# Kernel tuning notes

Measured on AMD Instinct MI355X. Metric: run time of the kernel, lower is better.

## Reference

```python
import jax, jax.numpy as jnp
import numpy as np

B, S, T = 2048, 32, 32
D, H = 128, 256       # cle_dim, rnn_dim
VS, VT = 256, 256     # source/target char vocab
BOW = 1               # MorphoDataset.Factor.BOW


def setup_inputs() -> dict:
    key = jax.random.key(0)
    ks = jax.random.split(key, 16)
    n = lambda k, sh: (jax.random.normal(k, sh, jnp.float32) * 0.05)
    inp = {
        "src_emb": n(ks[0], (VS, D)),
        "tgt_emb": n(ks[1], (VT, D)),
        "enc_f_W": n(ks[2], (D, 3 * H)),
        "enc_f_U": n(ks[3], (H, 3 * H)),
        "enc_f_b": jnp.zeros((2, 3 * H), jnp.float32),
        "enc_b_W": n(ks[4], (D, 3 * H)),
        "enc_b_U": n(ks[5], (H, 3 * H)),
        "enc_b_b": jnp.zeros((2, 3 * H), jnp.float32),
        "dec_W": n(ks[6], (D + H, 3 * H)),
        "dec_U": n(ks[7], (H, 3 * H)),
        "dec_b": jnp.zeros((2, 3 * H), jnp.float32),
        "out_W": n(ks[8], (H, VT)),
        "out_b": jnp.zeros((VT,), jnp.float32),
        "att_src_W": n(ks[9], (H, H)),
        "att_src_b": jnp.zeros((H,), jnp.float32),
        "att_st_W": n(ks[10], (H, H)),
        "att_st_b": jnp.zeros((H,), jnp.float32),
        "att_v": n(ks[11], (H, 1)),
        "att_v_b": jnp.zeros((1,), jnp.float32),
        "source_ids": jax.random.randint(ks[12], (B, S), 0, VS, jnp.int32),
        "target_ids": jax.random.randint(ks[13], (B, T), 0, VT, jnp.int32),
    }
    return inp


def _gru_step(h, x, W, U, b):
    # Keras GRU, reset_after=True: separate input/recurrent biases b[0], b[1]
    gx = x @ W + b[0]
    gh = h @ U + b[1]
    xz, xr, xh = jnp.split(gx, 3, axis=-1)
    hz, hr, hh = jnp.split(gh, 3, axis=-1)
    z = jax.nn.sigmoid(xz + hz)
    r = jax.nn.sigmoid(xr + hr)
    c = jnp.tanh(xh + r * hh)
    return z * h + (1.0 - z) * c


def _gru_scan(x_tbd, W, U, b):
    # x_tbd: [S, B, D] -> outputs [S, B, H]
    h0 = jnp.zeros((x_tbd.shape[1], U.shape[0]), x_tbd.dtype)
    def step(h, x):
        h = _gru_step(h, x, W, U, b)
        return h, h
    _, ys = jax.lax.scan(step, h0, x_tbd)
    return ys


def reference(src_emb, tgt_emb, enc_f_W, enc_f_U, enc_f_b, enc_b_W, enc_b_U, enc_b_b,
              dec_W, dec_U, dec_b, out_W, out_b, att_src_W, att_src_b,
              att_st_W, att_st_b, att_v, att_v_b, source_ids, target_ids):
    # ---- Encoder: bidirectional GRU, merge_mode='sum' ----
    x = src_emb[source_ids]                      # [B, S, D]
    x_t = jnp.transpose(x, (1, 0, 2))            # [S, B, D]
    fwd = _gru_scan(x_t, enc_f_W, enc_f_U, enc_f_b)
    bwd = _gru_scan(x_t[::-1], enc_b_W, enc_b_U, enc_b_b)[::-1]
    source_states = jnp.transpose(fwd + bwd, (1, 0, 2))  # [B, S, H]

    # projected source states are constant across decoder steps -> precompute
    proj_src = source_states @ att_src_W + att_src_b     # [B, S, H]

    def attend(inp, h):
        p = h @ att_st_W + att_st_b                      # [B, H]
        e = jnp.tanh(proj_src + p[:, None, :]) @ att_v + att_v_b  # [B, S, 1]
        w = jax.nn.softmax(e, axis=1)                    # softmax over source positions
        ctx = jnp.sum(source_states * w, axis=1)         # [B, H]
        return jnp.concatenate([inp, ctx], axis=1)       # [B, D+H]

    # ---- Decoder (teacher forcing) ----
    h0 = source_states[:, 0]                             # [B, H]
    bow = jnp.broadcast_to(tgt_emb[BOW], (source_ids.shape[0], tgt_emb.shape[1]))
    inp0 = attend(bow, h0)

    def dstep(carry, tgt_t):
        h, inp = carry
        h = _gru_step(h, inp, dec_W, dec_U, dec_b)       # GRUCell step
        logits = h @ out_W + out_b                       # [B, VT]
        nxt = attend(tgt_emb[tgt_t], h)
        return (h, nxt), logits

    _, logits = jax.lax.scan(dstep, (h0, inp0), jnp.transpose(target_ids))
    return jnp.transpose(logits, (1, 0, 2))              # [B, T, VT]
```

## Files before the change

kernel.cpp:

```cpp
#include <hip/hip_runtime.h>
#include <math.h>

#define B_  2048
#define S_  32
#define T_  32
#define D_  128
#define H_  256
#define G3  768
#define VT_ 256
#define BOW_ 1

typedef __attribute__((ext_vector_type(8))) short short8;
typedef __attribute__((ext_vector_type(4))) float f32x4;
typedef __attribute__((ext_vector_type(4))) unsigned short us4;
typedef __attribute__((ext_vector_type(8))) unsigned short us8;
typedef unsigned short u16;

__device__ inline u16 f2bf(float x) {
  union { float f; unsigned u; } v; v.f = x;
  unsigned r = v.u + 0x7FFFu + ((v.u >> 16) & 1u);
  return (u16)(r >> 16);
}
__device__ inline float bf2f(u16 b) {
  union { unsigned u; float f; } v; v.u = ((unsigned)b) << 16; return v.f;
}
__device__ inline int swz(int r) { return ((r ^ (r >> 3)) & 7) << 3; }
__device__ inline float sigm(float x) { return 1.f / (1.f + expf(-x)); }

struct TMat { const float* src; u16* dhi; u16* dlo; int R; int C; int tile0; };
struct TPack { TMat m[10]; };

__global__ __launch_bounds__(256)
void wsplit_t(TPack P) {
  int bx = blockIdx.x;
  TMat M = P.m[0];
  #pragma unroll
  for (int i = 1; i < 10; i++) if (bx >= P.m[i].tile0) M = P.m[i];
  int ti = bx - M.tile0;
  int tilesR = M.R >> 6;
  int rt = ti % tilesR, ct = ti / tilesR;
  int r0 = rt * 64, c0 = ct * 64;
  __shared__ float ts[64][65];
  int tid = threadIdx.x;
  int cx = tid & 63, ry = tid >> 6;
  #pragma unroll
  for (int i = 0; i < 16; i++) {
    int r = ry * 16 + i;
    ts[r][cx] = M.src[(size_t)(r0 + r) * M.C + c0 + cx];
  }
  __syncthreads();
  int rx = tid & 63, cy = tid >> 6;
  #pragma unroll
  for (int i = 0; i < 16; i++) {
    int cc = cy * 16 + i;
    float v = ts[rx][cc];
    u16 hi = f2bf(v);
    size_t o = (size_t)(c0 + cc) * M.R + r0 + rx;
    M.dhi[o] = hi;
    M.dlo[o] = f2bf(v - bf2f(hi));
  }
}

__global__ __launch_bounds__(256)
void esplit(const float* a, const float* b, u16* ah, u16* al, u16* bh, u16* bl, int n) {
  int i = blockIdx.x * 256 + threadIdx.x;
  if (i >= 2 * n) return;
  const float* s = (i < n) ? a : b;
  u16* dh = (i < n) ? ah : bh;
  u16* dl = (i < n) ? al : bl;
  int j = (i < n) ? i : i - n;
  float v = s[j];
  u16 hi = f2bf(v);
  dh[j] = hi; dl[j] = f2bf(v - bf2f(hi));
}

struct PLeg {
  const u16* Ahi; const u16* Alo; const float* Af32; int lda;
  const u16* Bthi; const u16* Btlo; int ldb;
  const float* bias; void* C; int ldc; int cmode;
  int M, N, K;
};

__global__ __launch_bounds__(256)
void gemm_pl(PLeg l0, PLeg l1) {
  PLeg L = blockIdx.z ? l1 : l0;
  int n0 = blockIdx.x * 128; if (n0 >= L.N) return;
  int m0 = blockIdx.y * 128; if (m0 >= L.M) return;
  __shared__ u16 As[128 * 64];
  __shared__ u16 Bs[128 * 64];
  int tid = threadIdx.x;
  int lane = tid & 63, wv = tid >> 6;
  int wr = (wv >> 1) * 64, wc = (wv & 1) * 64;
  int fr = lane & 15, fk = (lane >> 4) * 8;
  f32x4 acc[4][4];
  #pragma unroll
  for (int m = 0; m < 4; m++)
    #pragma unroll
    for (int n = 0; n < 4; n++) acc[m][n] = (f32x4){0.f, 0.f, 0.f, 0.f};

  int s_row = tid >> 1, s_part = tid & 1;

  for (int k0 = 0; k0 < L.K; k0 += 32) {
    if (k0) __syncthreads();
    int swA = swz(s_row);
    if (L.Af32) {
      const float* src = L.Af32 + (size_t)(m0 + s_row) * L.lda + k0 + s_part * 16;
      #pragma unroll
      for (int q = 0; q < 4; q++) {
        f32x4 v = *(const f32x4*)(src + q * 4);
        us4 hv, lv;
        #pragma unroll
        for (int j = 0; j < 4; j++) {
          u16 h = f2bf(v[j]); hv[j] = h; lv[j] = f2bf(v[j] - bf2f(h));
        }
        *(us4*)&As[(s_row * 64 + s_part * 16 + q * 4) ^ swA]      = hv;
        *(us4*)&As[(s_row * 64 + 32 + s_part * 16 + q * 4) ^ swA] = lv;
      }
    } else {
      const u16* src = (s_part ? L.Alo : L.Ahi) + (size_t)(m0 + s_row) * L.lda + k0;
      #pragma unroll
      for (int q = 0; q < 4; q++)
        *(us8*)&As[(s_row * 64 + s_part * 32 + q * 8) ^ swA] = *(const us8*)(src + q * 8);
    }
    {
      const u16* src = (s_part ? L.Btlo : L.Bthi) + (size_t)(n0 + s_row) * L.ldb + k0;
      #pragma unroll
      for (int q = 0; q < 4; q++)
        *(us8*)&Bs[(s_row * 64 + s_part * 32 + q * 8) ^ swA] = *(const us8*)(src + q * 8);
    }
    __syncthreads();
    short8 bhi[4], blo[4];
    #pragma unroll
    for (int n = 0; n < 4; n++) {
      int c = wc + n * 16 + fr; int sw = swz(c);
      bhi[n] = *(const short8*)&Bs[(c * 64 + fk) ^ sw];
      blo[n] = *(const short8*)&Bs[(c * 64 + 32 + fk) ^ sw];
    }
    #pragma unroll
    for (int m = 0; m < 4; m++) {
      int r = wr + m * 16 + fr; int sw = swz(r);
      short8 ahi = *(const short8*)&As[(r * 64 + fk) ^ sw];
      short8 alo = *(const short8*)&As[(r * 64 + 32 + fk) ^ sw];
      #pragma unroll
      for (int n = 0; n < 4; n++) {
        acc[m][n] = __builtin_amdgcn_mfma_f32_16x16x32_bf16(ahi, bhi[n], acc[m][n], 0, 0, 0);
        acc[m][n] = __builtin_amdgcn_mfma_f32_16x16x32_bf16(ahi, blo[n], acc[m][n], 0, 0, 0);
        acc[m][n] = __builtin_amdgcn_mfma_f32_16x16x32_bf16(alo, bhi[n], acc[m][n], 0, 0, 0);
      }
    }
  }
  int rbase = (lane >> 4) * 4;
  #pragma unroll
  for (int m = 0; m < 4; m++)
    #pragma unroll
    for (int rr = 0; rr < 4; rr++) {
      int row = m0 + wr + m * 16 + rbase + rr;
      #pragma unroll
      for (int n = 0; n < 4; n++) {
        int col = n0 + wc + n * 16 + fr;
        float v = acc[m][n][rr];
        if (L.bias) v += L.bias[col];
        if (L.cmode == 0) ((float*)L.C)[(size_t)row * L.ldc + col] = v;
        else              ((u16*)L.C)[(size_t)row * L.ldc + col] = f2bf(v);
      }
    }
}

struct Seg {
  const u16* Ahi; const u16* Alo; int lda;
  const u16* Bthi; const u16* Btlo; int ldb;
  int K; int gmode;
};
struct StepDesc {
  Seg seg[3]; int nseg;
  const float* b0; const float* b1;
  const float* hold; float* hnew;
  u16* hh; u16* hl;
  float* ssf; int ssmode;
  u16* ss0h; u16* ss0l; int writeSS0;
  const int* ids; int sidx;
};

__global__ __launch_bounds__(256)
void gru_step(StepDesc d0, StepDesc d1) {
  StepDesc D = blockIdx.z ? d1 : d0;
  int j0 = blockIdx.x * 64;
  int m0 = blockIdx.y * 64;
  __shared__ u16 As[64 * 64];
  __shared__ u16 Bs[3 * 64 * 64];
  int tid = threadIdx.x;
  int lane = tid & 63, wv = tid >> 6;
  int wr = (wv >> 1) * 32, wc = (wv & 1) * 32;
  int fr = lane & 15, fk = (lane >> 4) * 8;
  f32x4 acc[4][2][2];
  #pragma unroll
  for (int a = 0; a < 4; a++)
    #pragma unroll
    for (int m = 0; m < 2; m++)
      #pragma unroll
      for (int n = 0; n < 2; n++) acc[a][m][n] = (f32x4){0.f, 0.f, 0.f, 0.f};

  int a_row = tid >> 2, a_part = (tid >> 1) & 1, a_half = tid & 1;

  #pragma unroll
  for (int sg = 0; sg < 3; sg++) {
    if (sg < D.nseg) {
      Seg S = D.seg[sg];
      int grow = m0 + a_row;
      int arow;
      if (S.gmode == 0)      arow = grow;
      else if (S.gmode == 1) arow = D.ids[grow * S_ + D.sidx];
      else if (S.gmode == 2) arow = D.ids[grow * S_ + (S_ - 1 - D.sidx)];
      else                   arow = (D.sidx == 0) ? BOW_ : D.ids[grow * T_ + D.sidx - 1];
      const u16* Ap = a_part ? S.Alo : S.Ahi;
      for (int k0 = 0; k0 < S.K; k0 += 32) {
        if (!(sg == 0 && k0 == 0)) __syncthreads();
        {
          int sw = swz(a_row);
          const u16* src = Ap + (size_t)arow * S.lda + k0 + a_half * 16;
          int bse = a_row * 64 + a_part * 32 + a_half * 16;
          *(us8*)&As[(bse + 0) ^ sw] = *(const us8*)(src);
          *(us8*)&As[(bse + 8) ^ sw] = *(const us8*)(src + 8);
        }
        #pragma unroll
        for (int st = 0; st < 3; st++) {
          int n768 = st * H_ + j0 + a_row;
          const u16* srcB = (a_part ? S.Btlo : S.Bthi) + (size_t)n768 * S.ldb + k0 + a_half * 16;
          int sw = swz(a_row);
          int bse = a_row * 64 + a_part * 32 + a_half * 16;
          *(us8*)&Bs[st * 4096 + ((bse + 0) ^ sw)] = *(const us8*)(srcB);
          *(us8*)&Bs[st * 4096 + ((bse + 8) ^ sw)] = *(const us8*)(srcB + 8);
        }
        __syncthreads();
        short8 ah[2], al[2];
        #pragma unroll
        for (int m = 0; m < 2; m++) {
          int r = wr + m * 16 + fr; int sw = swz(r);
          ah[m] = *(const short8*)&As[(r * 64 + fk) ^ sw];
          al[m] = *(const short8*)&As[(r * 64 + 32 + fk) ^ sw];
        }
        #pragma unroll
        for (int st = 0; st < 3; st++) {
          int ai = (st < 2) ? st : (sg == 0 ? 2 : 3);
          #pragma unroll
          for (int n = 0; n < 2; n++) {
            int c = wc + n * 16 + fr; int sw = swz(c);
            short8 bh = *(const short8*)&Bs[st * 4096 + ((c * 64 + fk) ^ sw)];
            short8 bl = *(const short8*)&Bs[st * 4096 + ((c * 64 + 32 + fk) ^ sw)];
            #pragma unroll
            for (int m = 0; m < 2; m++) {
              acc[ai][m][n] = __builtin_amdgcn_mfma_f32_16x16x32_bf16(ah[m], bh, acc[ai][m][n], 0, 0, 0);
              acc[ai][m][n] = __builtin_amdgcn_mfma_f32_16x16x32_bf16(ah[m], bl, acc[ai][m][n], 0, 0, 0);
              acc[ai][m][n] = __builtin_amdgcn_mfma_f32_16x16x32_bf16(al[m], bh, acc[ai][m][n], 0, 0, 0);
            }
          }
        }
      }
    }
  }

  int rbase = (lane >> 4) * 4;
  #pragma unroll
  for (int m = 0; m < 2; m++)
    #pragma unroll
    for (int rr = 0; rr < 4; rr++) {
      int b = m0 + wr + m * 16 + rbase + rr;
      #pragma unroll
      for (int n = 0; n < 2; n++) {
        int j = j0 + wc + n * 16 + fr;
        float az  = acc[0][m][n][rr];
        float ar  = acc[1][m][n][rr];
        float ahc = acc[2][m][n][rr];
        float axc = acc[3][m][n][rr];
        float z = sigm(az + D.b0[j] + D.b1[j]);
        float r = sigm(ar + D.b0[H_ + j] + D.b1[H_ + j]);
        float c = tanhf(axc + D.b0[2 * H_ + j] + r * (ahc + D.b1[2 * H_ + j]));
        size_t o = (size_t)b * H_ + j;
        float hn = z * D.hold[o] + (1.f - z) * c;
        D.hnew[o] = hn;
        u16 hi = f2bf(hn);
        D.hh[o] = hi; D.hl[o] = f2bf(hn - bf2f(hi));
        if (D.ssmode == 1) {
          D.ssf[o] = hn;
        } else if (D.ssmode == 2) {
          float v = D.ssf[o] + hn;
          D.ssf[o] = v;
          if (D.writeSS0) {
            u16 vh = f2bf(v);
            D.ss0h[o] = vh; D.ss0l[o] = f2bf(v - bf2f(vh));
          }
        }
      }
    }
}

__global__ __launch_bounds__(256)
void attend_k(const u16* __restrict__ projbf, const float* __restrict__ ss,
              const float* __restrict__ p, const float* __restrict__ att_v,
              u16* __restrict__ ctxh, u16* __restrict__ ctxl) {
  int b = blockIdx.x;
  int tid = threadIdx.x;
  int lane = tid & 63;
  int wv = tid >> 6;
  __shared__ float e_s[S_];
  __shared__ float w_s[S_];
  float pq[4], vq[4];
  #pragma unroll
  for (int q = 0; q < 4; q++) {
    pq[q] = p[(size_t)b * H_ + q * 64 + lane];
    vq[q] = att_v[q * 64 + lane];
  }
  #pragma unroll
  for (int i = 0; i < 8; i++) {
    int s = wv * 8 + i;
    const u16* pr = projbf + ((size_t)s * B_ + b) * H_;
    float part = 0.f;
    #pragma unroll
    for (int q = 0; q < 4; q++)
      part += tanhf(bf2f(pr[q * 64 + lane]) + pq[q]) * vq[q];
    #pragma unroll
    for (int off = 32; off; off >>= 1)
      part += __shfl_xor(part, off);
    if (lane == 0) e_s[s] = part;
  }
  __syncthreads();
  float m = -1e30f;
  #pragma unroll
  for (int s = 0; s < S_; s++) m = fmaxf(m, e_s[s]);
  float den = 0.f;
  #pragma unroll
  for (int s = 0; s < S_; s++) den += expf(e_s[s] - m);
  if (tid < S_) w_s[tid] = expf(e_s[tid] - m) / den;
  __syncthreads();
  float acc = 0.f;
  #pragma unroll
  for (int s = 0; s < S_; s++)
    acc = fmaf(w_s[s], ss[((size_t)s * B_ + b) * H_ + tid], acc);
  u16 hi = f2bf(acc);
  size_t o = (size_t)b * H_ + tid;
  ctxh[o] = hi; ctxl[o] = f2bf(acc - bf2f(hi));
}

extern "C" void kernel_launch(void* const* d_in, const int* in_sizes, int n_in,
                              void* d_out, int out_size, void* d_ws, size_t ws_size,
                              hipStream_t stream) {
  const float* src_emb   = (const float*)d_in[0];
  const float* tgt_emb   = (const float*)d_in[1];
  const float* enc_f_W   = (const float*)d_in[2];
  const float* enc_f_U   = (const float*)d_in[3];
  const float* enc_f_b   = (const float*)d_in[4];
  const float* enc_b_W   = (const float*)d_in[5];
  const float* enc_b_U   = (const float*)d_in[6];
  const float* enc_b_b   = (const float*)d_in[7];
  const float* dec_W     = (const float*)d_in[8];
  const float* dec_U     = (const float*)d_in[9];
  const float* dec_b     = (const float*)d_in[10];
  const float* out_W     = (const float*)d_in[11];
  const float* out_b     = (const float*)d_in[12];
  const float* att_src_W = (const float*)d_in[13];
  const float* att_src_b = (const float*)d_in[14];
  const float* att_st_W  = (const float*)d_in[15];
  const float* att_st_b  = (const float*)d_in[16];
  const float* att_v     = (const float*)d_in[17];
  const int* source_ids  = (const int*)d_in[19];
  const int* target_ids  = (const int*)d_in[20];
  float* out = (float*)d_out;

  char* base = (char*)d_ws;
  size_t off = 0;
  auto allocB = [&](size_t bytes) { void* p = base + off; off = (off + bytes + 255) & ~255UL; return p; };
  const size_t BH = (size_t)B_ * H_;

  float* ss    = (float*)allocB((size_t)S_ * BH * 4);
  u16*  projbf = (u16*) allocB((size_t)S_ * BH * 2);
  float* pbuf  = (float*)allocB(BH * 4);
  u16* ctxh = (u16*)allocB(BH * 2);
  u16* ctxl = (u16*)allocB(BH * 2);
  u16* ss0h = (u16*)allocB(BH * 2);
  u16* ss0l = (u16*)allocB(BH * 2);
  float* hEncF[2][2]; u16* hEncH[2][2]; u16* hEncL[2][2];
  for (int d = 0; d < 2; d++)
    for (int p = 0; p < 2; p++) {
      hEncF[d][p] = (float*)allocB(BH * 4);
      hEncH[d][p] = (u16*)allocB(BH * 2);
      hEncL[d][p] = (u16*)allocB(BH * 2);
    }
  float* hDecF[2]; u16* hDecH[2]; u16* hDecL[2];
  for (int p = 0; p < 2; p++) {
    hDecF[p] = (float*)allocB(BH * 4);
    hDecH[p] = (u16*)allocB(BH * 2);
    hDecL[p] = (u16*)allocB(BH * 2);
  }
  auto planes2 = [&](size_t n, u16*& h, u16*& l) { h = (u16*)allocB(n * 2); l = (u16*)allocB(n * 2); };
  u16 *UtFh,*UtFl,*UtBh,*UtBl,*WtFh,*WtFl,*WtBh,*WtBl;
  u16 *dUth,*dUtl,*dWcth,*dWctl,*dWxth,*dWxtl;
  u16 *oWth,*oWtl,*aStth,*aSttl,*aSrth,*aSrtl;
  u16 *sEh,*sEl,*tEh,*tEl;
  planes2((size_t)G3*H_, UtFh, UtFl);   planes2((size_t)G3*H_, UtBh, UtBl);
  planes2((size_t)G3*D_, WtFh, WtFl);   planes2((size_t)G3*D_, WtBh, WtBl);
  planes2((size_t)G3*H_, dUth, dUtl);   planes2((size_t)G3*H_, dWcth, dWctl);
  planes2((size_t)G3*D_, dWxth, dWxtl);
  planes2((size_t)H_*VT_, oWth, oWtl);
  planes2((size_t)H_*H_, aStth, aSttl); planes2((size_t)H_*H_, aSrth, aSrtl);
  planes2((size_t)VT_*D_, sEh, sEl);    planes2((size_t)VT_*D_, tEh, tEl);

  TPack P;
  P.m[0] = { enc_f_U,            UtFh, UtFl, 256, 768, 0   };
  P.m[1] = { enc_b_U,            UtBh, UtBl, 256, 768, 48  };
  P.m[2] = { dec_U,              dUth, dUtl, 256, 768, 96  };
  P.m[3] = { dec_W + 128 * G3,   dWcth, dWctl, 256, 768, 144 };
  P.m[4] = { enc_f_W,            WtFh, WtFl, 128, 768, 192 };
  P.m[5] = { enc_b_W,            WtBh, WtBl, 128, 768, 216 };
  P.m[6] = { dec_W,              dWxth, dWxtl, 128, 768, 240 };
  P.m[7] = { out_W,              oWth, oWtl, 256, 256, 264 };
  P.m[8] = { att_st_W,           aStth, aSttl, 256, 256, 280 };
  P.m[9] = { att_src_W,          aSrth, aSrtl, 256, 256, 296 };
  wsplit_t<<<312, 256, 0, stream>>>(P);
  esplit<<<(2 * VT_ * D_ + 255) / 256, 256, 0, stream>>>(src_emb, tgt_emb, sEh, sEl, tEh, tEl, VT_ * D_);

  for (int d = 0; d < 2; d++) {
    hipMemsetAsync(hEncF[d][0], 0, BH * 4, stream);
    hipMemsetAsync(hEncH[d][0], 0, BH * 2, stream);
    hipMemsetAsync(hEncL[d][0], 0, BH * 2, stream);
  }

  for (int s = 0; s < S_; s++) {
    int p = s & 1;
    StepDesc dd[2];
    for (int d = 0; d < 2; d++) {
      StepDesc& D = dd[d];
      D.seg[0] = { hEncH[d][p], hEncL[d][p], H_, d ? UtBh : UtFh, d ? UtBl : UtFl, H_, H_, 0 };
      D.seg[1] = { sEh, sEl, D_, d ? WtBh : WtFh, d ? WtBl : WtFl, D_, D_, d ? 2 : 1 };
      D.seg[2] = D.seg[1];
      D.nseg = 2;
      D.b0 = d ? enc_b_b : enc_f_b;
      D.b1 = (d ? enc_b_b : enc_f_b) + G3;
      D.hold = hEncF[d][p]; D.hnew = hEncF[d][p ^ 1];
      D.hh = hEncH[d][p ^ 1]; D.hl = hEncL[d][p ^ 1];
      int pos = d ? (S_ - 1 - s) : s;
      D.ssf = ss + (size_t)pos * BH;
      D.ssmode = (s < S_ / 2) ? 1 : 2;
      D.ss0h = ss0h; D.ss0l = ss0l;
      D.writeSS0 = (d == 1 && s == S_ - 1) ? 1 : 0;
      D.ids = source_ids; D.sidx = s;
    }
    gru_step<<<dim3(4, 32, 2), 256, 0, stream>>>(dd[0], dd[1]);
  }

  {
    PLeg proj = { nullptr, nullptr, ss, H_, aSrth, aSrtl, H_, att_src_b,
                  projbf, H_, 1, S_ * B_, H_, H_ };
    PLeg p0   = { nullptr, nullptr, ss, H_, aStth, aSttl, H_, att_st_b,
                  pbuf, H_, 0, B_, H_, H_ };
    gemm_pl<<<dim3(2, 512, 2), 256, 0, stream>>>(proj, p0);
  }
  attend_k<<<B_, 256, 0, stream>>>(projbf, ss, pbuf, att_v, ctxh, ctxl);

  for (int t = 0; t < T_; t++) {
    int p = t & 1;
    StepDesc D;
    D.seg[0] = { t ? hDecH[p] : ss0h, t ? hDecL[p] : ss0l, H_, dUth, dUtl, H_, H_, 0 };
    D.seg[1] = { ctxh, ctxl, H_, dWcth, dWctl, H_, H_, 0 };
    D.seg[2] = { tEh, tEl, D_, dWxth, dWxtl, D_, D_, 3 };
    D.nseg = 3;
    D.b0 = dec_b; D.b1 = dec_b + G3;
    D.hold = t ? hDecF[p] : ss;
    D.hnew = hDecF[p ^ 1];
    D.hh = hDecH[p ^ 1]; D.hl = hDecL[p ^ 1];
    D.ssf = nullptr; D.ssmode = 0;
    D.ss0h = nullptr; D.ss0l = nullptr; D.writeSS0 = 0;
    D.ids = target_ids; D.sidx = t;
    gru_step<<<dim3(4, 32, 1), 256, 0, stream>>>(D, D);

    PLeg LO = { hDecH[p ^ 1], hDecL[p ^ 1], nullptr, H_, oWth, oWtl, H_, out_b,
                out + (size_t)t * VT_, T_ * VT_, 0, B_, VT_, H_ };
    PLeg LP = { hDecH[p ^ 1], hDecL[p ^ 1], nullptr, H_, aStth, aSttl, H_, att_st_b,
                pbuf, H_, 0, B_, H_, H_ };
    gemm_pl<<<dim3(2, 16, 2), 256, 0, stream>>>(LO, LP);

    if (t < T_ - 1)
      attend_k<<<B_, 256, 0, stream>>>(projbf, ss, pbuf, att_v, ctxh, ctxl);
  }
}
```

Measured before the change: 4.048 ms.

## Restructure GRU step kernel and batch decoder output projection after the loop

The GRU step kernel now stages the whole concatenated A operand (hidden state, context and embedding rows) in shared memory once, with 32-row tiles. B weights are streamed directly from global memory instead of being staged per k-chunk through LDS, which removes most barriers. Source states are kept as bf16 hi/lo planes instead of fp32. All decoder hidden states are stored so the output logits projection runs as one large GEMM after the loop rather than once per step. This cuts per-step launch work and synchronisation, but B loads now hit global or cache memory with no LDS reuse, and attention now uses only the bf16 high part of the source states, which lowers its precision.

```diff
diff --git a/kernel.cpp b/kernel.cpp
--- a/kernel.cpp
+++ b/kernel.cpp
@@ -12,7 +12,6 @@
 
 typedef __attribute__((ext_vector_type(8))) short short8;
 typedef __attribute__((ext_vector_type(4))) float f32x4;
-typedef __attribute__((ext_vector_type(4))) unsigned short us4;
 typedef __attribute__((ext_vector_type(8))) unsigned short us8;
 typedef unsigned short u16;
 
@@ -75,7 +74,7 @@
 }
 
 struct PLeg {
-  const u16* Ahi; const u16* Alo; const float* Af32; int lda;
+  const u16* Ahi; const u16* Alo; int lda;
   const u16* Bthi; const u16* Btlo; int ldb;
   const float* bias; void* C; int ldc; int cmode;
   int M, N, K;
@@ -103,20 +102,7 @@
   for (int k0 = 0; k0 < L.K; k0 += 32) {
     if (k0) __syncthreads();
     int swA = swz(s_row);
-    if (L.Af32) {
-      const float* src = L.Af32 + (size_t)(m0 + s_row) * L.lda + k0 + s_part * 16;
-      #pragma unroll
-      for (int q = 0; q < 4; q++) {
-        f32x4 v = *(const f32x4*)(src + q * 4);
-        us4 hv, lv;
-        #pragma unroll
-        for (int j = 0; j < 4; j++) {
-          u16 h = f2bf(v[j]); hv[j] = h; lv[j] = f2bf(v[j] - bf2f(h));
-        }
-        *(us4*)&As[(s_row * 64 + s_part * 16 + q * 4) ^ swA]      = hv;
-        *(us4*)&As[(s_row * 64 + 32 + s_part * 16 + q * 4) ^ swA] = lv;
-      }
-    } else {
+    {
       const u16* src = (s_part ? L.Alo : L.Ahi) + (size_t)(m0 + s_row) * L.lda + k0;
       #pragma unroll
       for (int q = 0; q < 4; q++)
@@ -160,142 +146,159 @@
         int col = n0 + wc + n * 16 + fr;
         float v = acc[m][n][rr];
         if (L.bias) v += L.bias[col];
-        if (L.cmode == 0) ((float*)L.C)[(size_t)row * L.ldc + col] = v;
-        else              ((u16*)L.C)[(size_t)row * L.ldc + col] = f2bf(v);
-      }
-    }
-}
-
-struct Seg {
-  const u16* Ahi; const u16* Alo; int lda;
-  const u16* Bthi; const u16* Btlo; int ldb;
-  int K; int gmode;
+        if (L.cmode == 0)      ((float*)L.C)[(size_t)row * L.ldc + col] = v;
+        else if (L.cmode == 1) ((u16*)L.C)[(size_t)row * L.ldc + col] = f2bf(v);
+        else {
+          size_t o = (((size_t)(row & (B_ - 1))) * T_ + (row >> 11)) * VT_ + col;
+          ((float*)L.C)[o] = v;
+        }
+      }
+    }
+}
+
+struct GruDesc {
+  const u16 *a0H, *a0L;
+  const u16 *a1H, *a1L;
+  const u16 *a2H, *a2L;
+  const u16 *b0H, *b0L;
+  const u16 *b1H, *b1L;
+  const u16 *b2H, *b2L;
+  const float *bias0, *bias1;
+  const float *hold;
+  const u16 *holdH, *holdL;
+  float *hnew;
+  u16 *hh, *hl;
+  u16 *ssH, *ssL;
+  const int *ids;
+  int ssmode;
+  int sidx, rev;
 };
-struct StepDesc {
-  Seg seg[3]; int nseg;
-  const float* b0; const float* b1;
-  const float* hold; float* hnew;
-  u16* hh; u16* hl;
-  float* ssf; int ssmode;
-  u16* ss0h; u16* ss0l; int writeSS0;
-  const int* ids; int sidx;
-};
-
+
+template<int MODE>
 __global__ __launch_bounds__(256)
-void gru_step(StepDesc d0, StepDesc d1) {
-  StepDesc D = blockIdx.z ? d1 : d0;
+void gru_step(GruDesc d0, GruDesc d1) {
+  GruDesc D = blockIdx.z ? d1 : d0;
+  constexpr int KT  = MODE ? 640 : 384;
+  constexpr int KT8 = KT / 8;
+  __shared__ u16 As[2 * 32 * KT];
+
   int j0 = blockIdx.x * 64;
-  int m0 = blockIdx.y * 64;
-  __shared__ u16 As[64 * 64];
-  __shared__ u16 Bs[3 * 64 * 64];
+  int m0 = blockIdx.y * 32;
   int tid = threadIdx.x;
   int lane = tid & 63, wv = tid >> 6;
-  int wr = (wv >> 1) * 32, wc = (wv & 1) * 32;
-  int fr = lane & 15, fk = (lane >> 4) * 8;
-  f32x4 acc[4][2][2];
+  int fr = lane & 15, kq = lane >> 4;
+  int jn = j0 + wv * 16 + fr;
+
+  constexpr int SLOTS = 2 * 32 * KT8;
+  constexpr int PER_T = SLOTS / 256;
+  #pragma unroll
+  for (int i = 0; i < PER_T; i++) {
+    int s = tid + i * 256;
+    int p = s / (32 * KT8);
+    int rem = s - p * (32 * KT8);
+    int row = rem / KT8;
+    int kb = rem - row * KT8;
+    int k = kb * 8;
+    const u16* src;
+    if (MODE == 0) {
+      if (k < 256) src = (p ? D.a0L : D.a0H) + (size_t)(m0 + row) * 256 + k;
+      else {
+        int ar = D.ids[(m0 + row) * S_ + (D.rev ? (S_ - 1 - D.sidx) : D.sidx)];
+        src = (p ? D.a1L : D.a1H) + (size_t)ar * 128 + (k - 256);
+      }
+    } else {
+      if (k < 256)      src = (p ? D.a0L : D.a0H) + (size_t)(m0 + row) * 256 + k;
+      else if (k < 512) src = (p ? D.a1L : D.a1H) + (size_t)(m0 + row) * 256 + (k - 256);
+      else {
+        int ar = (D.sidx == 0) ? BOW_ : D.ids[(m0 + row) * T_ + D.sidx - 1];
+        src = (p ? D.a2L : D.a2H) + (size_t)ar * 128 + (k - 512);
+      }
+    }
+    *(us8*)&As[(s ^ (row & 7)) * 8] = *(const us8*)src;
+  }
+  __syncthreads();
+
+  f32x4 acc[4][2];
   #pragma unroll
   for (int a = 0; a < 4; a++)
     #pragma unroll
-    for (int m = 0; m < 2; m++)
+    for (int m = 0; m < 2; m++) acc[a][m] = (f32x4){0.f, 0.f, 0.f, 0.f};
+
+  int arow_slot[2];
+  #pragma unroll
+  for (int m = 0; m < 2; m++) arow_slot[m] = (m * 16 + fr) * KT8 + kq;
+
+  auto kstep = [&](int k0, int bk, const u16* bHp, const u16* bLp, int ldb, int ai2) {
+    short8 ah[2], al[2];
+    #pragma unroll
+    for (int m = 0; m < 2; m++) {
+      int sl = (arow_slot[m] + (k0 >> 3)) ^ (fr & 7);
+      ah[m] = *(const short8*)&As[sl * 8];
+      sl = (arow_slot[m] + 32 * KT8 + (k0 >> 3)) ^ (fr & 7);
+      al[m] = *(const short8*)&As[sl * 8];
+    }
+    #pragma unroll
+    for (int st = 0; st < 3; st++) {
+      size_t ro = (size_t)(st * 256 + jn) * ldb + bk + kq * 8;
+      short8 bh = *(const short8*)(bHp + ro);
+      short8 bl = *(const short8*)(bLp + ro);
+      int ai = (st < 2) ? st : ai2;
       #pragma unroll
-      for (int n = 0; n < 2; n++) acc[a][m][n] = (f32x4){0.f, 0.f, 0.f, 0.f};
-
-  int a_row = tid >> 2, a_part = (tid >> 1) & 1, a_half = tid & 1;
-
-  #pragma unroll
-  for (int sg = 0; sg < 3; sg++) {
-    if (sg < D.nseg) {
-      Seg S = D.seg[sg];
-      int grow = m0 + a_row;
-      int arow;
-      if (S.gmode == 0)      arow = grow;
-      else if (S.gmode == 1) arow = D.ids[grow * S_ + D.sidx];
-      else if (S.gmode == 2) arow = D.ids[grow * S_ + (S_ - 1 - D.sidx)];
-      else                   arow = (D.sidx == 0) ? BOW_ : D.ids[grow * T_ + D.sidx - 1];
-      const u16* Ap = a_part ? S.Alo : S.Ahi;
-      for (int k0 = 0; k0 < S.K; k0 += 32) {
-        if (!(sg == 0 && k0 == 0)) __syncthreads();
-        {
-          int sw = swz(a_row);
-          const u16* src = Ap + (size_t)arow * S.lda + k0 + a_half * 16;
-          int bse = a_row * 64 + a_part * 32 + a_half * 16;
-          *(us8*)&As[(bse + 0) ^ sw] = *(const us8*)(src);
-          *(us8*)&As[(bse + 8) ^ sw] = *(const us8*)(src + 8);
+      for (int m = 0; m < 2; m++) {
+        acc[ai][m] = __builtin_amdgcn_mfma_f32_16x16x32_bf16(ah[m], bh, acc[ai][m], 0, 0, 0);
+        acc[ai][m] = __builtin_amdgcn_mfma_f32_16x16x32_bf16(ah[m], bl, acc[ai][m], 0, 0, 0);
+        acc[ai][m] = __builtin_amdgcn_mfma_f32_16x16x32_bf16(al[m], bh, acc[ai][m], 0, 0, 0);
+      }
+    }
+  };
+
+  #pragma unroll
+  for (int k0 = 0; k0 < 256; k0 += 32) kstep(k0, k0, D.b0H, D.b0L, 256, 2);
+  if (MODE == 0) {
+    #pragma unroll
+    for (int k0 = 256; k0 < 384; k0 += 32) kstep(k0, k0 - 256, D.b1H, D.b1L, 128, 3);
+  } else {
+    #pragma unroll
+    for (int k0 = 256; k0 < 512; k0 += 32) kstep(k0, k0 - 256, D.b1H, D.b1L, 256, 3);
+    #pragma unroll
+    for (int k0 = 512; k0 < 640; k0 += 32) kstep(k0, k0 - 512, D.b2H, D.b2L, 128, 3);
+  }
+
+  int rbase = kq * 4;
+  int j = jn;
+  float bz = D.bias0[j] + D.bias1[j];
+  float br = D.bias0[H_ + j] + D.bias1[H_ + j];
+  float bxc = D.bias0[2 * H_ + j];
+  float bhc = D.bias1[2 * H_ + j];
+  #pragma unroll
+  for (int m = 0; m < 2; m++)
+    #pragma unroll
+    for (int rr = 0; rr < 4; rr++) {
+      int b = m0 + m * 16 + rbase + rr;
+      size_t o = (size_t)b * H_ + j;
+      float z = sigm(acc[0][m][rr] + bz);
+      float r = sigm(acc[1][m][rr] + br);
+      float c = tanhf(acc[3][m][rr] + bxc + r * (acc[2][m][rr] + bhc));
+      float hprev = D.hold ? D.hold[o] : (bf2f(D.holdH[o]) + bf2f(D.holdL[o]));
+      float hn = z * hprev + (1.f - z) * c;
+      D.hnew[o] = hn;
+      u16 hi = f2bf(hn);
+      D.hh[o] = hi; D.hl[o] = f2bf(hn - bf2f(hi));
+      if (MODE == 0) {
+        if (D.ssmode == 1) {
+          u16 vh = f2bf(hn);
+          D.ssH[o] = vh; D.ssL[o] = f2bf(hn - bf2f(vh));
+        } else if (D.ssmode == 2) {
+          float v = bf2f(D.ssH[o]) + bf2f(D.ssL[o]) + hn;
+          u16 vh = f2bf(v);
+          D.ssH[o] = vh; D.ssL[o] = f2bf(v - bf2f(vh));
         }
-        #pragma unroll
-        for (int st = 0; st < 3; st++) {
-          int n768 = st * H_ + j0 + a_row;
-          const u16* srcB = (a_part ? S.Btlo : S.Bthi) + (size_t)n768 * S.ldb + k0 + a_half * 16;
-          int sw = swz(a_row);
-          int bse = a_row * 64 + a_part * 32 + a_half * 16;
-          *(us8*)&Bs[st * 4096 + ((bse + 0) ^ sw)] = *(const us8*)(srcB);
-          *(us8*)&Bs[st * 4096 + ((bse + 8) ^ sw)] = *(const us8*)(srcB + 8);
-        }
-        __syncthreads();
-        short8 ah[2], al[2];
-        #pragma unroll
-        for (int m = 0; m < 2; m++) {
-          int r = wr + m * 16 + fr; int sw = swz(r);
-          ah[m] = *(const short8*)&As[(r * 64 + fk) ^ sw];
-          al[m] = *(const short8*)&As[(r * 64 + 32 + fk) ^ sw];
-        }
-        #pragma unroll
-        for (int st = 0; st < 3; st++) {
-          int ai = (st < 2) ? st : (sg == 0 ? 2 : 3);
-          #pragma unroll
-          for (int n = 0; n < 2; n++) {
-            int c = wc + n * 16 + fr; int sw = swz(c);
-            short8 bh = *(const short8*)&Bs[st * 4096 + ((c * 64 + fk) ^ sw)];
-            short8 bl = *(const short8*)&Bs[st * 4096 + ((c * 64 + 32 + fk) ^ sw)];
-            #pragma unroll
-            for (int m = 0; m < 2; m++) {
-              acc[ai][m][n] = __builtin_amdgcn_mfma_f32_16x16x32_bf16(ah[m], bh, acc[ai][m][n], 0, 0, 0);
-              acc[ai][m][n] = __builtin_amdgcn_mfma_f32_16x16x32_bf16(ah[m], bl, acc[ai][m][n], 0, 0, 0);
-              acc[ai][m][n] = __builtin_amdgcn_mfma_f32_16x16x32_bf16(al[m], bh, acc[ai][m][n], 0, 0, 0);
-            }
-          }
-        }
-      }
-    }
-  }
-
-  int rbase = (lane >> 4) * 4;
-  #pragma unroll
-  for (int m = 0; m < 2; m++)
-    #pragma unroll
-    for (int rr = 0; rr < 4; rr++) {
-      int b = m0 + wr + m * 16 + rbase + rr;
-      #pragma unroll
-      for (int n = 0; n < 2; n++) {
-        int j = j0 + wc + n * 16 + fr;
-        float az  = acc[0][m][n][rr];
-        float ar  = acc[1][m][n][rr];
-        float ahc = acc[2][m][n][rr];
-        float axc = acc[3][m][n][rr];
-        float z = sigm(az + D.b0[j] + D.b1[j]);
-        float r = sigm(ar + D.b0[H_ + j] + D.b1[H_ + j]);
-        float c = tanhf(axc + D.b0[2 * H_ + j] + r * (ahc + D.b1[2 * H_ + j]));
-        size_t o = (size_t)b * H_ + j;
-        float hn = z * D.hold[o] + (1.f - z) * c;
-        D.hnew[o] = hn;
-        u16 hi = f2bf(hn);
-        D.hh[o] = hi; D.hl[o] = f2bf(hn - bf2f(hi));
-        if (D.ssmode == 1) {
-          D.ssf[o] = hn;
-        } else if (D.ssmode == 2) {
-          float v = D.ssf[o] + hn;
-          D.ssf[o] = v;
-          if (D.writeSS0) {
-            u16 vh = f2bf(v);
-            D.ss0h[o] = vh; D.ss0l[o] = f2bf(v - bf2f(vh));
-          }
-        }
       }
     }
 }
 
 __global__ __launch_bounds__(256)
-void attend_k(const u16* __restrict__ projbf, const float* __restrict__ ss,
+void attend_k(const u16* __restrict__ projbf, const u16* __restrict__ ssH,
               const float* __restrict__ p, const float* __restrict__ att_v,
               u16* __restrict__ ctxh, u16* __restrict__ ctxl) {
   int b = blockIdx.x;
@@ -335,7 +338,7 @@
   float acc = 0.f;
   #pragma unroll
   for (int s = 0; s < S_; s++)
-    acc = fmaf(w_s[s], ss[((size_t)s * B_ + b) * H_ + tid], acc);
+    acc = fmaf(w_s[s], bf2f(ssH[((size_t)s * B_ + b) * H_ + tid]), acc);
   u16 hi = f2bf(acc);
   size_t o = (size_t)b * H_ + tid;
   ctxh[o] = hi; ctxl[o] = f2bf(acc - bf2f(hi));
@@ -371,26 +374,25 @@
   auto allocB = [&](size_t bytes) { void* p = base + off; off = (off + bytes + 255) & ~255UL; return p; };
   const size_t BH = (size_t)B_ * H_;
 
-  float* ss    = (float*)allocB((size_t)S_ * BH * 4);
-  u16*  projbf = (u16*) allocB((size_t)S_ * BH * 2);
-  float* pbuf  = (float*)allocB(BH * 4);
+  u16* ssH    = (u16*)allocB((size_t)S_ * BH * 2);
+  u16* ssL    = (u16*)allocB((size_t)S_ * BH * 2);
+  u16* projbf = (u16*)allocB((size_t)S_ * BH * 2);
+  float* pbuf = (float*)allocB(BH * 4);
   u16* ctxh = (u16*)allocB(BH * 2);
   u16* ctxl = (u16*)allocB(BH * 2);
-  u16* ss0h = (u16*)allocB(BH * 2);
-  u16* ss0l = (u16*)allocB(BH * 2);
-  float* hEncF[2][2]; u16* hEncH[2][2]; u16* hEncL[2][2];
-  for (int d = 0; d < 2; d++)
-    for (int p = 0; p < 2; p++) {
-      hEncF[d][p] = (float*)allocB(BH * 4);
-      hEncH[d][p] = (u16*)allocB(BH * 2);
-      hEncL[d][p] = (u16*)allocB(BH * 2);
-    }
-  float* hDecF[2]; u16* hDecH[2]; u16* hDecL[2];
-  for (int p = 0; p < 2; p++) {
-    hDecF[p] = (float*)allocB(BH * 4);
-    hDecH[p] = (u16*)allocB(BH * 2);
-    hDecL[p] = (u16*)allocB(BH * 2);
-  }
+
+  float* encF0 = (float*)allocB(2 * BH * 4);
+  u16*  encPl0 = (u16*)allocB(4 * BH * 2);
+  float* encF1 = (float*)allocB(2 * BH * 4);
+  u16*  encPl1 = (u16*)allocB(4 * BH * 2);
+  float* encF[2][2]  = { { encF0, encF0 + BH }, { encF1, encF1 + BH } };
+  u16*  encH[2][2]   = { { encPl0, encPl0 + 2 * BH }, { encPl1, encPl1 + 2 * BH } };
+  u16*  encL[2][2]   = { { encPl0 + BH, encPl0 + 3 * BH }, { encPl1 + BH, encPl1 + 3 * BH } };
+
+  float* hDecF[2] = { (float*)allocB(BH * 4), (float*)allocB(BH * 4) };
+  u16* hAllH = (u16*)allocB((size_t)T_ * BH * 2);
+  u16* hAllL = (u16*)allocB((size_t)T_ * BH * 2);
+
   auto planes2 = [&](size_t n, u16*& h, u16*& l) { h = (u16*)allocB(n * 2); l = (u16*)allocB(n * 2); };
   u16 *UtFh,*UtFl,*UtBh,*UtBl,*WtFh,*WtFl,*WtBh,*WtBl;
   u16 *dUth,*dUtl,*dWcth,*dWctl,*dWxth,*dWxtl;
@@ -405,80 +407,84 @@
   planes2((size_t)VT_*D_, sEh, sEl);    planes2((size_t)VT_*D_, tEh, tEl);
 
   TPack P;
-  P.m[0] = { enc_f_U,            UtFh, UtFl, 256, 768, 0   };
-  P.m[1] = { enc_b_U,            UtBh, UtBl, 256, 768, 48  };
-  P.m[2] = { dec_U,              dUth, dUtl, 256, 768, 96  };
-  P.m[3] = { dec_W + 128 * G3,   dWcth, dWctl, 256, 768, 144 };
-  P.m[4] = { enc_f_W,            WtFh, WtFl, 128, 768, 192 };
-  P.m[5] = { enc_b_W,            WtBh, WtBl, 128, 768, 216 };
-  P.m[6] = { dec_W,              dWxth, dWxtl, 128, 768, 240 };
-  P.m[7] = { out_W,              oWth, oWtl, 256, 256, 264 };
-  P.m[8] = { att_st_W,           aStth, aSttl, 256, 256, 280 };
-  P.m[9] = { att_src_W,          aSrth, aSrtl, 256, 256, 296 };
+  P.m[0] = { enc_f_U,          UtFh, UtFl, 256, 768, 0   };
+  P.m[1] = { enc_b_U,          UtBh, UtBl, 256, 768, 48  };
+  P.m[2] = { dec_U,            dUth, dUtl, 256, 768, 96  };
+  P.m[3] = { dec_W + 128 * G3, dWcth, dWctl, 256, 768, 144 };
+  P.m[4] = { enc_f_W,          WtFh, WtFl, 128, 768, 192 };
+  P.m[5] = { enc_b_W,          WtBh, WtBl, 128, 768, 216 };
+  P.m[6] = { dec_W,            dWxth, dWxtl, 128, 768, 240 };
+  P.m[7] = { out_W,            oWth, oWtl, 256, 256, 264 };
+  P.m[8] = { att_st_W,         aStth, aSttl, 256, 256, 280 };
+  P.m[9] = { att_src_W,        aSrth, aSrtl, 256, 256, 296 };
   wsplit_t<<<312, 256, 0, stream>>>(P);
   esplit<<<(2 * VT_ * D_ + 255) / 256, 256, 0, stream>>>(src_emb, tgt_emb, sEh, sEl, tEh, tEl, VT_ * D_);
 
-  for (int d = 0; d < 2; d++) {
-    hipMemsetAsync(hEncF[d][0], 0, BH * 4, stream);
-    hipMemsetAsync(hEncH[d][0], 0, BH * 2, stream);
-    hipMemsetAsync(hEncL[d][0], 0, BH * 2, stream);
-  }
+  hipMemsetAsync(encF0, 0, 2 * BH * 4, stream);
+  hipMemsetAsync(encPl0, 0, 4 * BH * 2, stream);
 
   for (int s = 0; s < S_; s++) {
     int p = s & 1;
-    StepDesc dd[2];
+    GruDesc dd[2];
     for (int d = 0; d < 2; d++) {
-      StepDesc& D = dd[d];
-      D.seg[0] = { hEncH[d][p], hEncL[d][p], H_, d ? UtBh : UtFh, d ? UtBl : UtFl, H_, H_, 0 };
-      D.seg[1] = { sEh, sEl, D_, d ? WtBh : WtFh, d ? WtBl : WtFl, D_, D_, d ? 2 : 1 };
-      D.seg[2] = D.seg[1];
-      D.nseg = 2;
-      D.b0 = d ? enc_b_b : enc_f_b;
-      D.b1 = (d ? enc_b_b : enc_f_b) + G3;
-      D.hold = hEncF[d][p]; D.hnew = hEncF[d][p ^ 1];
-      D.hh = hEncH[d][p ^ 1]; D.hl = hEncL[d][p ^ 1];
+      GruDesc& D = dd[d];
+      D.a0H = encH[p][d]; D.a0L = encL[p][d];
+      D.a1H = sEh; D.a1L = sEl;
+      D.a2H = nullptr; D.a2L = nullptr;
+      D.b0H = d ? UtBh : UtFh; D.b0L = d ? UtBl : UtFl;
+      D.b1H = d ? WtBh : WtFh; D.b1L = d ? WtBl : WtFl;
+      D.b2H = nullptr; D.b2L = nullptr;
+      D.bias0 = d ? enc_b_b : enc_f_b;
+      D.bias1 = (d ? enc_b_b : enc_f_b) + G3;
+      D.hold = encF[p][d]; D.holdH = nullptr; D.holdL = nullptr;
+      D.hnew = encF[p ^ 1][d];
+      D.hh = encH[p ^ 1][d]; D.hl = encL[p ^ 1][d];
       int pos = d ? (S_ - 1 - s) : s;
-      D.ssf = ss + (size_t)pos * BH;
+      D.ssH = ssH + (size_t)pos * BH; D.ssL = ssL + (size_t)pos * BH;
+      D.ids = source_ids;
       D.ssmode = (s < S_ / 2) ? 1 : 2;
-      D.ss0h = ss0h; D.ss0l = ss0l;
-      D.writeSS0 = (d == 1 && s == S_ - 1) ? 1 : 0;
-      D.ids = source_ids; D.sidx = s;
-    }
-    gru_step<<<dim3(4, 32, 2), 256, 0, stream>>>(dd[0], dd[1]);
+      D.sidx = s; D.rev = d;
+    }
+    gru_step<0><<<dim3(4, 64, 2), 256, 0, stream>>>(dd[0], dd[1]);
   }
 
   {
-    PLeg proj = { nullptr, nullptr, ss, H_, aSrth, aSrtl, H_, att_src_b,
-                  projbf, H_, 1, S_ * B_, H_, H_ };
-    PLeg p0   = { nullptr, nullptr, ss, H_, aStth, aSttl, H_, att_st_b,
-                  pbuf, H_, 0, B_, H_, H_ };
+    PLeg proj = { ssH, ssL, H_, aSrth, aSrtl, H_, att_src_b, projbf, H_, 1, S_ * B_, H_, H_ };
+    PLeg p0   = { ssH, ssL, H_, aStth, aSttl, H_, att_st_b,  pbuf,   H_, 0, B_,      H_, H_ };
     gemm_pl<<<dim3(2, 512, 2), 256, 0, stream>>>(proj, p0);
   }
-  attend_k<<<B_, 256, 0, stream>>>(projbf, ss, pbuf, att_v, ctxh, ctxl);
+  attend_k<<<B_, 256, 0, stream>>>(projbf, ssH, pbuf, att_v, ctxh, ctxl);
 
   for (int t = 0; t < T_; t++) {
     int p = t & 1;
-    StepDesc D;
-    D.seg[0] = { t ? hDecH[p] : ss0h, t ? hDecL[p] : ss0l, H_, dUth, dUtl, H_, H_, 0 };
-    D.seg[1] = { ctxh, ctxl, H_, dWcth, dWctl, H_, H_, 0 };
-    D.seg[2] = { tEh, tEl, D_, dWxth, dWxtl, D_, D_, 3 };
-    D.nseg = 3;
-    D.b0 = dec_b; D.b1 = dec_b + G3;
-    D.hold = t ? hDecF[p] : ss;
+    GruDesc D = {};
+    D.a0H = t ? hAllH + (size_t)(t - 1) * BH : ssH;
+    D.a0L = t ? hAllL + (size_t)(t - 1) * BH : ssL;
+    D.a1H = ctxh; D.a1L = ctxl;
+    D.a2H = tEh;  D.a2L = tEl;
+    D.b0H = dUth;  D.b0L = dUtl;
+    D.b1H = dWcth; D.b1L = dWctl;
+    D.b2H = dWxth; D.b2L = dWxtl;
+    D.bias0 = dec_b; D.bias1 = dec_b + G3;
+    if (t == 0) { D.hold = nullptr; D.holdH = ssH; D.holdL = ssL; }
+    else        { D.hold = hDecF[p]; D.holdH = nullptr; D.holdL = nullptr; }
     D.hnew = hDecF[p ^ 1];
-    D.hh = hDecH[p ^ 1]; D.hl = hDecL[p ^ 1];
-    D.ssf = nullptr; D.ssmode = 0;
-    D.ss0h = nullptr; D.ss0l = nullptr; D.writeSS0 = 0;
-    D.ids = target_ids; D.sidx = t;
-    gru_step<<<dim3(4, 32, 1), 256, 0, stream>>>(D, D);
-
-    PLeg LO = { hDecH[p ^ 1], hDecL[p ^ 1], nullptr, H_, oWth, oWtl, H_, out_b,
-                out + (size_t)t * VT_, T_ * VT_, 0, B_, VT_, H_ };
-    PLeg LP = { hDecH[p ^ 1], hDecL[p ^ 1], nullptr, H_, aStth, aSttl, H_, att_st_b,
-                pbuf, H_, 0, B_, H_, H_ };
-    gemm_pl<<<dim3(2, 16, 2), 256, 0, stream>>>(LO, LP);
-
-    if (t < T_ - 1)
-      attend_k<<<B_, 256, 0, stream>>>(projbf, ss, pbuf, att_v, ctxh, ctxl);
-  }
-}
+    D.hh = hAllH + (size_t)t * BH; D.hl = hAllL + (size_t)t * BH;
+    D.ssH = nullptr; D.ssL = nullptr;
+    D.ids = target_ids;
+    D.ssmode = 0; D.sidx = t; D.rev = 0;
+    gru_step<1><<<dim3(4, 64, 1), 256, 0, stream>>>(D, D);
+
+    if (t < T_ - 1) {
+      PLeg LP = { hAllH + (size_t)t * BH, hAllL + (size_t)t * BH, H_,
+                  aStth, aSttl, H_, att_st_b, pbuf, H_, 0, B_, H_, H_ };
+      gemm_pl<<<dim3(2, 16, 1), 256, 0, stream>>>(LP, LP);
+      attend_k<<<B_, 256, 0, stream>>>(projbf, ssH, pbuf, att_v, ctxh, ctxl);
+    }
+  }
+
+  {
+    PLeg LO = { hAllH, hAllL, H_, oWth, oWtl, H_, out_b, out, 0, 2, T_ * B_, VT_, H_ };
+    gemm_pl<<<dim3(2, 512, 1), 256, 0, stream>>>(LO, LO);
+  }
+}
```

After: 3.648 ms. -9.9%, faster.
